# Kernel optimization log

Hardware: AMD Instinct MI355X
Metric: run time of the kernel (lower is better)

The kernel has to match this reference:

```python
import jax, jax.numpy as jnp
import numpy as np
from jax import lax

BN_EPS = 1e-5


def _conv(x, w, b, stride):
    # x: [N,C,H,W], w: [O,I,3,3], stride 2, padding 1
    y = lax.conv_general_dilated(
        x, w, window_strides=(stride, stride), padding=((1, 1), (1, 1)),
        dimension_numbers=('NCHW', 'OIHW', 'NCHW'))
    return y + b[None, :, None, None]


def _batchnorm(x, gamma, beta):
    # training-mode BN: batch statistics over (N,H,W)
    mean = jnp.mean(x, axis=(0, 2, 3), keepdims=True)
    var = jnp.var(x, axis=(0, 2, 3), keepdims=True)
    xn = (x - mean) * lax.rsqrt(var + BN_EPS)
    return xn * gamma[None, :, None, None] + beta[None, :, None, None]


def _maxpool2(x):
    return lax.reduce_window(x, -jnp.inf, lax.max, (1, 1, 2, 2), (1, 1, 2, 2), 'VALID')


def setup_inputs() -> dict:
    key = jax.random.key(0)
    ks = jax.random.split(key, 8)
    B, C, H, W = 128, 3, 224, 224
    x = jax.random.normal(ks[0], (B, C, H, W), dtype=jnp.float32)
    conv1_w = jax.random.normal(ks[1], (16, 3, 3, 3), dtype=jnp.float32) * (1.0 / np.sqrt(3 * 9))
    conv1_b = jnp.zeros((16,), dtype=jnp.float32)
    bn1_g = jnp.ones((16,), dtype=jnp.float32)
    bn1_b = jnp.zeros((16,), dtype=jnp.float32)
    conv2_w = jax.random.normal(ks[2], (32, 16, 3, 3), dtype=jnp.float32) * (1.0 / np.sqrt(16 * 9))
    conv2_b = jnp.zeros((32,), dtype=jnp.float32)
    bn2_g = jnp.ones((32,), dtype=jnp.float32)
    bn2_b = jnp.zeros((32,), dtype=jnp.float32)
    fc_w = jax.random.normal(ks[3], (1, 32), dtype=jnp.float32) * (1.0 / np.sqrt(32))
    fc_b = jnp.zeros((1,), dtype=jnp.float32)
    return dict(x=x, conv1_w=conv1_w, conv1_b=conv1_b, bn1_g=bn1_g, bn1_b=bn1_b,
                conv2_w=conv2_w, conv2_b=conv2_b, bn2_g=bn2_g, bn2_b=bn2_b,
                fc_w=fc_w, fc_b=fc_b)


def reference(x, conv1_w, conv1_b, bn1_g, bn1_b, conv2_w, conv2_b, bn2_g, bn2_b, fc_w, fc_b):
    h = jax.nn.relu(_batchnorm(_conv(x, conv1_w, conv1_b, 2), bn1_g, bn1_b))   # [B,16,112,112]
    h = _maxpool2(h)                                                           # [B,16,56,56]
    h = jax.nn.relu(_batchnorm(_conv(h, conv2_w, conv2_b, 2), bn2_g, bn2_b))   # [B,32,28,28]
    h = jnp.mean(h, axis=(2, 3))                                               # AdaptiveAvgPool2d((1,1)) -> [B,32]
    logits = h @ fc_w.T + fc_b                                                 # [B,1]
    # Quantum circuit: RY(theta) on all wires, CNOT chain, <Z_0>.
    # Z on the control wire commutes with every CNOT -> expval = cos(theta).
    probs = jnp.cos(logits)                                                    # [B,1]
    return jnp.concatenate((probs, 1.0 - probs), axis=-1)                      # [B,2]
```

## Files before the change

kernel.cpp:

```cpp
#include <hip/hip_runtime.h>
#include <math.h>

#define BATCH 128
#define CIN 3
#define H 224
#define W 224
#define C1 16
#define HP 56
#define WP 56
#define C2 32
#define H2 28
#define W2 28

__global__ __launch_bounds__(256) void conv1_fused_k(
    const float* __restrict__ x, const float* __restrict__ w1,
    const float* __restrict__ b1, float2* __restrict__ mm,
    float* __restrict__ s_sum, float* __restrict__ s_sq)
{
    __shared__ float red[4][8], redq[4][8];
    const int tid = threadIdx.x;
    const int t = blockIdx.x * 256 + tid;
    const int c0 = blockIdx.y * 8;
    const int n = t / 3136;
    const int r = t % 3136;
    const int ph = r / 56;
    const int pw = r % 56;
    const int rbase = 4 * ph - 1;
    const int cbase = 4 * pw;
    const bool topok = ph > 0;
    const bool pwok  = pw > 0;

    float acc[8][4];
#pragma unroll
    for (int j = 0; j < 8; ++j) {
        const float bb = b1[c0 + j];
#pragma unroll
        for (int q = 0; q < 4; ++q) acc[j][q] = bb;
    }

#pragma unroll
    for (int ci = 0; ci < CIN; ++ci) {
        const float* img = x + (n * CIN + ci) * (H * W);
#pragma unroll
        for (int l = 0; l < 5; ++l) {
            const int ih = max(rbase + l, 0);
            const float* rowp = img + ih * W;
            const float4 f4 = *(const float4*)(rowp + cbase);
            const float lf = rowp[max(cbase - 1, 0)];
            const bool rok = (l > 0) || topok;
            const float p0 = (rok && pwok) ? lf : 0.0f;
            const float p1 = rok ? f4.x : 0.0f;
            const float p2 = rok ? f4.y : 0.0f;
            const float p3 = rok ? f4.z : 0.0f;
            const float p4 = rok ? f4.w : 0.0f;
#pragma unroll
            for (int j = 0; j < 8; ++j) {
                const float* wc = w1 + ((c0 + j) * CIN + ci) * 9;
                if (l < 3) {
                    const float wa = wc[l * 3 + 0];
                    const float wb = wc[l * 3 + 1];
                    const float wd = wc[l * 3 + 2];
                    acc[j][0] += wa * p0 + wb * p1 + wd * p2;
                    acc[j][1] += wa * p2 + wb * p3 + wd * p4;
                }
                if (l >= 2) {
                    const int kh = l - 2;
                    const float wa = wc[kh * 3 + 0];
                    const float wb = wc[kh * 3 + 1];
                    const float wd = wc[kh * 3 + 2];
                    acc[j][2] += wa * p0 + wb * p1 + wd * p2;
                    acc[j][3] += wa * p2 + wb * p3 + wd * p4;
                }
            }
        }
    }

#pragma unroll
    for (int j = 0; j < 8; ++j) {
        const int o = (n * C1 + c0 + j) * (HP * WP) + ph * WP + pw;
        const float a0 = acc[j][0], a1 = acc[j][1], a2 = acc[j][2], a3 = acc[j][3];
        mm[o] = make_float2(fmaxf(fmaxf(a0, a1), fmaxf(a2, a3)),
                            fminf(fminf(a0, a1), fminf(a2, a3)));
        float s = a0 + a1 + a2 + a3;
        float q = a0 * a0 + a1 * a1 + a2 * a2 + a3 * a3;
#pragma unroll
        for (int off = 32; off > 0; off >>= 1) {
            s += __shfl_xor(s, off);
            q += __shfl_xor(q, off);
        }
        if ((tid & 63) == 0) { red[tid >> 6][j] = s; redq[tid >> 6][j] = q; }
    }
    __syncthreads();
    if (tid < 8) {
        atomicAdd(&s_sum[c0 + tid],
                  red[0][tid] + red[1][tid] + red[2][tid] + red[3][tid]);
    } else if (tid < 16) {
        const int j = tid - 8;
        atomicAdd(&s_sq[c0 + j],
                  redq[0][j] + redq[1][j] + redq[2][j] + redq[3][j]);
    }
}

__global__ __launch_bounds__(256) void conv2_k(
    const float2* __restrict__ mm,
    const float* __restrict__ s1sum, const float* __restrict__ s1sq,
    const float* __restrict__ g1, const float* __restrict__ be1,
    const float* __restrict__ w2, const float* __restrict__ b2,
    float* __restrict__ y2,
    float* __restrict__ s_sum, float* __restrict__ s_sq)
{
    __shared__ float red[4][8], redq[4][8];
    const int tid = threadIdx.x;
    const int t = blockIdx.x * 256 + tid;
    const int c0 = blockIdx.y * 8;
    const int n = t / 392;
    const int r = t % 392;
    const int oh = r / 14;
    const int ow = (r % 14) * 2;
    const bool topok = oh > 0;
    const bool owok  = ow > 0;
    const float inv1 = 1.0f / (float)(BATCH * 112 * 112);

    float accA[8], accB[8];
#pragma unroll
    for (int c = 0; c < 8; ++c) { accA[c] = b2[c0 + c]; accB[c] = accA[c]; }

#pragma unroll 2
    for (int ci = 0; ci < C1; ++ci) {
        const float mean = s1sum[ci] * inv1;
        const float var  = s1sq[ci] * inv1 - mean * mean;
        const float s1 = g1[ci] * rsqrtf(var + 1e-5f);
        const float t1 = be1[ci] - mean * s1;

        const float2* pl = mm + (n * C1 + ci) * (HP * WP);

        float4 fa[3], fb[3];
        float2 lpv[3];
#pragma unroll
        for (int kh = 0; kh < 3; ++kh) {
            const int ih = max(2 * oh - 1 + kh, 0);
            const float2* rowp = pl + ih * WP;
            fa[kh]  = *(const float4*)(rowp + 2 * ow);
            fb[kh]  = *(const float4*)(rowp + 2 * ow + 2);
            lpv[kh] = rowp[max(2 * ow - 1, 0)];
        }

        float h[3][5];
#pragma unroll
        for (int kh = 0; kh < 3; ++kh) {
            const bool rok = (kh > 0) || topok;
            const float u0 = fmaxf(0.0f, fmaxf(s1 * lpv[kh].x + t1, s1 * lpv[kh].y + t1));
            const float u1 = fmaxf(0.0f, fmaxf(s1 * fa[kh].x + t1, s1 * fa[kh].y + t1));
            const float u2 = fmaxf(0.0f, fmaxf(s1 * fa[kh].z + t1, s1 * fa[kh].w + t1));
            const float u3 = fmaxf(0.0f, fmaxf(s1 * fb[kh].x + t1, s1 * fb[kh].y + t1));
            const float u4 = fmaxf(0.0f, fmaxf(s1 * fb[kh].z + t1, s1 * fb[kh].w + t1));
            h[kh][0] = (rok && owok) ? u0 : 0.0f;
            h[kh][1] = rok ? u1 : 0.0f;
            h[kh][2] = rok ? u2 : 0.0f;
            h[kh][3] = rok ? u3 : 0.0f;
            h[kh][4] = rok ? u4 : 0.0f;
        }

#pragma unroll
        for (int c = 0; c < 8; ++c) {
            const float* wc = w2 + ((c0 + c) * C1 + ci) * 9;
            float a = accA[c], b = accB[c];
#pragma unroll
            for (int kh = 0; kh < 3; ++kh) {
                const float w0 = wc[kh * 3 + 0];
                const float w1v = wc[kh * 3 + 1];
                const float w2v = wc[kh * 3 + 2];
                a += w0 * h[kh][0] + w1v * h[kh][1] + w2v * h[kh][2];
                b += w0 * h[kh][2] + w1v * h[kh][3] + w2v * h[kh][4];
            }
            accA[c] = a; accB[c] = b;
        }
    }

#pragma unroll
    for (int c = 0; c < 8; ++c) {
        const float aA = accA[c], aB = accB[c];
        const int p = oh * W2 + ow;
        *(float2*)(y2 + (n * C2 + c0 + c) * (H2 * W2) + p) = make_float2(aA, aB);
        float s = aA + aB, q = aA * aA + aB * aB;
#pragma unroll
        for (int off = 32; off > 0; off >>= 1) {
            s += __shfl_xor(s, off);
            q += __shfl_xor(q, off);
        }
        if ((tid & 63) == 0) { red[tid >> 6][c] = s; redq[tid >> 6][c] = q; }
    }
    __syncthreads();
    if (tid < 8) {
        atomicAdd(&s_sum[c0 + tid],
                  red[0][tid] + red[1][tid] + red[2][tid] + red[3][tid]);
    } else if (tid < 16) {
        const int c = tid - 8;
        atomicAdd(&s_sq[c0 + c],
                  redq[0][c] + redq[1][c] + redq[2][c] + redq[3][c]);
    }
}

__global__ __launch_bounds__(256) void head_fused_k(
    const float* __restrict__ y2,
    const float* __restrict__ s2sum, const float* __restrict__ s2sq,
    const float* __restrict__ g2, const float* __restrict__ be2,
    const float* __restrict__ fcw, const float* __restrict__ fcb,
    float* __restrict__ out)
{
    __shared__ float feat[C2];
    const int n = blockIdx.x;
    const int tid = threadIdx.x;
    const int wave = tid >> 6, lane = tid & 63;
    const float inv2 = 1.0f / (float)(BATCH * H2 * W2);
#pragma unroll
    for (int k = 0; k < 8; ++k) {
        const int c = wave * 8 + k;
        const float mean = s2sum[c] * inv2;
        const float var  = s2sq[c] * inv2 - mean * mean;
        const float s = g2[c] * rsqrtf(var + 1e-5f);
        const float t = be2[c] - mean * s;
        const float4* yp = (const float4*)(y2 + (n * C2 + c) * (H2 * W2));
        float a = 0.0f;
        for (int i = lane; i < 196; i += 64) {
            const float4 v = yp[i];
            a += fmaxf(0.0f, s * v.x + t) + fmaxf(0.0f, s * v.y + t)
               + fmaxf(0.0f, s * v.z + t) + fmaxf(0.0f, s * v.w + t);
        }
#pragma unroll
        for (int off = 32; off > 0; off >>= 1) a += __shfl_xor(a, off);
        if (lane == 0) feat[c] = a * (1.0f / (H2 * W2));
    }
    __syncthreads();
    if (tid == 0) {
        float logit = fcb[0];
#pragma unroll
        for (int c = 0; c < C2; ++c) logit += feat[c] * fcw[c];
        const float pc = cosf(logit);
        out[2 * n]     = pc;
        out[2 * n + 1] = 1.0f - pc;
    }
}

extern "C" void kernel_launch(void* const* d_in, const int* in_sizes, int n_in,
                              void* d_out, int out_size, void* d_ws, size_t ws_size,
                              hipStream_t stream) {
    const float* x   = (const float*)d_in[0];
    const float* w1  = (const float*)d_in[1];
    const float* b1  = (const float*)d_in[2];
    const float* g1  = (const float*)d_in[3];
    const float* be1 = (const float*)d_in[4];
    const float* w2  = (const float*)d_in[5];
    const float* b2  = (const float*)d_in[6];
    const float* g2  = (const float*)d_in[7];
    const float* be2 = (const float*)d_in[8];
    const float* fcw = (const float*)d_in[9];
    const float* fcb = (const float*)d_in[10];
    float* out = (float*)d_out;

    float* ws = (float*)d_ws;
    float2* mm = (float2*)ws;
    float* y2 = ws + (size_t)2 * BATCH * C1 * HP * WP;
    float* stats = y2 + (size_t)BATCH * C2 * H2 * W2;
    float* s1sum = stats;
    float* s1sq  = stats + 16;
    float* s2sum = stats + 32;
    float* s2sq  = stats + 64;

    hipMemsetAsync(stats, 0, 96 * sizeof(float), stream);

    conv1_fused_k<<<dim3(1568, 2), 256, 0, stream>>>(x, w1, b1, mm, s1sum, s1sq);
    conv2_k<<<dim3(196, 4), 256, 0, stream>>>(mm, s1sum, s1sq, g1, be1,
                                              w2, b2, y2, s2sum, s2sq);
    head_fused_k<<<BATCH, 256, 0, stream>>>(y2, s2sum, s2sq, g2, be2,
                                            fcw, fcb, out);
}
```

Baseline: 230.7 us.

## Stage conv1 input rows in LDS via direct global-to-LDS loads, compute all 16 channels

Conv1 now gives each block one image and a band of four pooled rows. The needed 17 input rows per channel are copied into shared memory with global_load_lds DMA instructions, and each thread computes all 16 output channels instead of 8. This stops two separate blocks from reading the same input for the two channel halves, and turns the overlapping strided global reads into LDS reads. In exchange it adds a large shared tile (about 45 KB), which lowers occupancy, uses more accumulator registers, and leaves 8 of 64 lanes idle per wave.

```diff
diff --git a/kernel.cpp b/kernel.cpp
--- a/kernel.cpp
+++ b/kernel.cpp
@@ -12,50 +12,75 @@
 #define H2 28
 #define W2 28
 
+#define TROWS 17
+#define CHF (TROWS * W)
+#define CHB (CHF * 4)
+
 __global__ __launch_bounds__(256) void conv1_fused_k(
     const float* __restrict__ x, const float* __restrict__ w1,
     const float* __restrict__ b1, float2* __restrict__ mm,
     float* __restrict__ s_sum, float* __restrict__ s_sq)
 {
-    __shared__ float red[4][8], redq[4][8];
+    __shared__ __align__(16) float tile[3 * CHF];
+    __shared__ float red[4][16], redq[4][16];
+
     const int tid = threadIdx.x;
-    const int t = blockIdx.x * 256 + tid;
-    const int c0 = blockIdx.y * 8;
-    const int n = t / 3136;
-    const int r = t % 3136;
-    const int ph = r / 56;
-    const int pw = r % 56;
-    const int rbase = 4 * ph - 1;
-    const int cbase = 4 * pw;
+    const int wave = tid >> 6, lane = tid & 63;
+    const int bid = blockIdx.x;
+    const int n = bid / 14;
+    const int g = bid % 14;
+    const int ph0 = g * 4;
+    const int ph = ph0 + wave;
+    const int pw = (lane < 56) ? lane : 55;
+    const bool active = lane < 56;
     const bool topok = ph > 0;
     const bool pwok  = pw > 0;
 
-    float acc[8][4];
-#pragma unroll
-    for (int j = 0; j < 8; ++j) {
-        const float bb = b1[c0 + j];
+    const int startrow = (g == 0) ? 0 : (4 * ph0 - 1);
+    const int nops     = (g == 0) ? 14 : 15;
+    const int base_off = (g == 0) ? (W * 4) : 0;
+#pragma unroll
+    for (int ci = 0; ci < CIN; ++ci) {
+        const char* gch = (const char*)(x + ((size_t)n * CIN + ci) * (H * W)
+                                        + (size_t)startrow * W);
+        char* lch = (char*)tile + ci * CHB + base_off;
+        for (int kp = wave; kp < nops; kp += 4) {
+            int off = kp * 1024;
+            if (off > 14208) off = 14208;
+            __builtin_amdgcn_global_load_lds(
+                (const __attribute__((address_space(1))) void*)(gch + off + lane * 16),
+                (__attribute__((address_space(3))) void*)(lch + off),
+                16, 0, 0);
+        }
+    }
+
+    float acc[16][4];
+#pragma unroll
+    for (int j = 0; j < 16; ++j) {
+        const float bb = b1[j];
 #pragma unroll
         for (int q = 0; q < 4; ++q) acc[j][q] = bb;
     }
 
+    __syncthreads();
+
 #pragma unroll
     for (int ci = 0; ci < CIN; ++ci) {
-        const float* img = x + (n * CIN + ci) * (H * W);
 #pragma unroll
         for (int l = 0; l < 5; ++l) {
-            const int ih = max(rbase + l, 0);
-            const float* rowp = img + ih * W;
-            const float4 f4 = *(const float4*)(rowp + cbase);
-            const float lf = rowp[max(cbase - 1, 0)];
+            const int tr = 4 * wave + l;
+            const float* rp = tile + ci * CHF + tr * W;
+            const float4 fa = *(const float4*)(rp + 4 * pw);
+            const float4 fb = *(const float4*)(rp + max(4 * pw - 4, 0));
             const bool rok = (l > 0) || topok;
-            const float p0 = (rok && pwok) ? lf : 0.0f;
-            const float p1 = rok ? f4.x : 0.0f;
-            const float p2 = rok ? f4.y : 0.0f;
-            const float p3 = rok ? f4.z : 0.0f;
-            const float p4 = rok ? f4.w : 0.0f;
-#pragma unroll
-            for (int j = 0; j < 8; ++j) {
-                const float* wc = w1 + ((c0 + j) * CIN + ci) * 9;
+            const float p0 = (rok && pwok) ? fb.w : 0.0f;
+            const float p1 = rok ? fa.x : 0.0f;
+            const float p2 = rok ? fa.y : 0.0f;
+            const float p3 = rok ? fa.z : 0.0f;
+            const float p4 = rok ? fa.w : 0.0f;
+#pragma unroll
+            for (int j = 0; j < 16; ++j) {
+                const float* wc = w1 + (j * CIN + ci) * 9;
                 if (l < 3) {
                     const float wa = wc[l * 3 + 0];
                     const float wb = wc[l * 3 + 1];
@@ -76,27 +101,29 @@
     }
 
 #pragma unroll
-    for (int j = 0; j < 8; ++j) {
-        const int o = (n * C1 + c0 + j) * (HP * WP) + ph * WP + pw;
+    for (int j = 0; j < 16; ++j) {
         const float a0 = acc[j][0], a1 = acc[j][1], a2 = acc[j][2], a3 = acc[j][3];
-        mm[o] = make_float2(fmaxf(fmaxf(a0, a1), fmaxf(a2, a3)),
-                            fminf(fminf(a0, a1), fminf(a2, a3)));
-        float s = a0 + a1 + a2 + a3;
-        float q = a0 * a0 + a1 * a1 + a2 * a2 + a3 * a3;
+        if (active) {
+            const int o = (n * C1 + j) * (HP * WP) + ph * WP + pw;
+            mm[o] = make_float2(fmaxf(fmaxf(a0, a1), fmaxf(a2, a3)),
+                                fminf(fminf(a0, a1), fminf(a2, a3)));
+        }
+        float s = active ? (a0 + a1 + a2 + a3) : 0.0f;
+        float q = active ? (a0 * a0 + a1 * a1 + a2 * a2 + a3 * a3) : 0.0f;
 #pragma unroll
         for (int off = 32; off > 0; off >>= 1) {
             s += __shfl_xor(s, off);
             q += __shfl_xor(q, off);
         }
-        if ((tid & 63) == 0) { red[tid >> 6][j] = s; redq[tid >> 6][j] = q; }
+        if (lane == 0) { red[wave][j] = s; redq[wave][j] = q; }
     }
     __syncthreads();
-    if (tid < 8) {
-        atomicAdd(&s_sum[c0 + tid],
+    if (tid < 16) {
+        atomicAdd(&s_sum[tid],
                   red[0][tid] + red[1][tid] + red[2][tid] + red[3][tid]);
-    } else if (tid < 16) {
-        const int j = tid - 8;
-        atomicAdd(&s_sq[c0 + j],
+    } else if (tid < 32) {
+        const int j = tid - 16;
+        atomicAdd(&s_sq[j],
                   redq[0][j] + redq[1][j] + redq[2][j] + redq[3][j]);
     }
 }
@@ -269,7 +296,7 @@
 
     hipMemsetAsync(stats, 0, 96 * sizeof(float), stream);
 
-    conv1_fused_k<<<dim3(1568, 2), 256, 0, stream>>>(x, w1, b1, mm, s1sum, s1sq);
+    conv1_fused_k<<<dim3(1792), 256, 0, stream>>>(x, w1, b1, mm, s1sum, s1sq);
     conv2_k<<<dim3(196, 4), 256, 0, stream>>>(mm, s1sum, s1sq, g1, be1,
                                               w2, b2, y2, s2sum, s2sq);
     head_fused_k<<<BATCH, 256, 0, stream>>>(y2, s2sum, s2sq, g2, be2,
```

Result: faster. 219.8 us (-4.7%).
